# Optimization experiments

Hardware: AMD Instinct MI355X
Metric: run time of the kernel (lower is better)

The kernel has to match this reference:

```python
import jax, jax.numpy as jnp
from jax import lax
import numpy as np

B, T, F = 4096, 512, 63
NOINPUTS, HIDDEN, OUT = 64, 1024, 1  # NOINPUTS = F + OUT


def setup_inputs() -> dict:
    key = jax.random.key(0)
    k1, k2, k3, k4, k5, k6 = jax.random.split(key, 6)
    inputs = jax.random.normal(k1, (B, T, F), dtype=jnp.float32)
    labels = jax.random.normal(k2, (B, T, 1), dtype=jnp.float32)
    # FFNN params: Linear(noinputs, hidden) -> ReLU -> Linear(hidden, out)
    s1 = 1.0 / np.sqrt(NOINPUTS)
    s2 = 1.0 / np.sqrt(HIDDEN)
    W1 = jax.random.uniform(k3, (NOINPUTS, HIDDEN), jnp.float32, -s1, s1)
    b1 = jax.random.uniform(k4, (HIDDEN,), jnp.float32, -s1, s1)
    W2 = jax.random.uniform(k5, (HIDDEN, OUT), jnp.float32, -s2, s2)
    b2 = jax.random.uniform(k6, (OUT,), jnp.float32, -s2, s2)
    return {"inputs": inputs, "labels": labels, "W1": W1, "b1": b1, "W2": W2, "b2": b2}


def reference(inputs, labels, W1, b1, W2, b2):
    # output_size == 1 branch: result tensor starts as zeros (B,1,1);
    # each step feeds [inputs[:,t,:], last_pred] through the MLP.
    Bb = inputs.shape[0]

    def step(prev_pred, x_t):  # prev_pred: (B,1), x_t: (B,F)
        mi = jnp.concatenate([x_t, prev_pred], axis=1)      # (B, noinputs)
        h = jax.nn.relu(mi @ W1 + b1)                        # (B, hidden)
        pred = h @ W2 + b2                                   # (B, 1)
        return pred, pred

    xs = jnp.swapaxes(inputs[:, 1:, :], 0, 1)                # (T-1, B, F)
    init = jnp.zeros((Bb, 1), inputs.dtype)
    _, preds = lax.scan(step, init, xs)                      # (T-1, B, 1)
    preds = jnp.swapaxes(preds, 0, 1)                        # (B, T-1, 1)
    zero0 = jnp.zeros((Bb, 1, 1), inputs.dtype)
    return jnp.concatenate([zero0, preds], axis=1)           # (B, T, 1)
```

## Files before the change

### kernel.cpp

```cpp
#include <hip/hip_runtime.h>


#define TT 512
#define FF 63
#define HID 1024

typedef __attribute__((ext_vector_type(4))) float f32x4;
typedef __attribute__((ext_vector_type(4))) int i32x4;
typedef __attribute__((ext_vector_type(8))) _Float16 h16x8;

struct __attribute__((packed, aligned(4))) uf2 { float x, y; };

__device__ __forceinline__ void lds_barrier() {
  asm volatile("s_waitcnt lgkmcnt(0)" ::: "memory");
  __builtin_amdgcn_s_barrier();
  asm volatile("" ::: "memory");
}

__device__ __forceinline__ int pkh(float a, float b) {
  auto h = __builtin_amdgcn_cvt_pkrtz(fmaxf(a, 0.f), fmaxf(b, 0.f));
  return __builtin_bit_cast(int, h);
}
__device__ __forceinline__ int pk2h(float a, float b) {
  auto h = __builtin_amdgcn_cvt_pkrtz(a, b);
  return __builtin_bit_cast(int, h);
}

__global__ __launch_bounds__(512, 2)
void ffnn_ar_kernel(const float* __restrict__ x,
                    const float* __restrict__ W1,
                    const float* __restrict__ b1,
                    const float* __restrict__ W2,
                    const float* __restrict__ b2p,
                    float* __restrict__ out) {
  __shared__ __align__(16) _Float16 lds_A[2][16][72];
  __shared__ __align__(16) float lds_part[2][16][12];

  const int tid  = threadIdx.x;
  const int lane = tid & 63;
  const int w    = tid >> 6;
  const int c    = lane & 15;
  const int g    = lane >> 4;
  const int br   = blockIdx.x * 16;

  h16x8 bfr[8][2];
#pragma unroll
  for (int i = 0; i < 8; ++i) {
    const int n = (w * 8 + i) * 16 + c;
#pragma unroll
    for (int ks = 0; ks < 2; ++ks) {
      h16x8 f;
#pragma unroll
      for (int j = 0; j < 8; ++j) f[j] = (_Float16)W1[(ks * 32 + g * 8 + j) * HID + n];
      bfr[i][ks] = f;
    }
  }
  f32x4 b1v[8], w63v[8];
#pragma unroll
  for (int i = 0; i < 8; ++i) {
    const int nb = (w * 8 + i) * 16 + g * 4;
    b1v[i]  = (f32x4){b1[nb], b1[nb + 1], b1[nb + 2], b1[nb + 3]};
    w63v[i] = (f32x4){W1[63 * HID + nb], W1[63 * HID + nb + 1],
                      W1[63 * HID + nb + 2], W1[63 * HID + nb + 3]};
  }
  h16x8 a2f[4];
#pragma unroll
  for (int i2 = 0; i2 < 4; ++i2) {
    h16x8 f;
#pragma unroll
    for (int j = 0; j < 8; ++j)
      f[j] = (_Float16)W2[(w * 8 + 2 * i2 + (j >> 2)) * 16 + g * 4 + (j & 3)];
    a2f[i2] = f;
  }
  const float b2 = b2p[0];
  const float b2w = (w == 0) ? b2 : 0.f;

  const int srow = tid >> 5;
  const int sl   = tid & 31;
  const long rowbase = (long)(br + srow) * (TT * FF);
  const bool full = (sl < 31);

  {
    float xa, xb;
    if (full) { const uf2 v = *reinterpret_cast<const uf2*>(&x[rowbase + FF + 2 * sl]); xa = v.x; xb = v.y; }
    else      { xa = x[rowbase + FF + 62]; xb = 0.f; }
    *reinterpret_cast<int*>(&lds_A[1][srow][2 * sl]) = pk2h(xa, xb);
  }
  if (tid < 384) reinterpret_cast<float*>(lds_part)[tid] = 0.f;
  if (tid < 16) out[(long)(br + tid) * TT] = 0.f;

  float s0a, s0b, s1a, s1b;
  if (full) {
    const uf2 v0 = *reinterpret_cast<const uf2*>(&x[rowbase + 2 * FF + 2 * sl]);
    const uf2 v1 = *reinterpret_cast<const uf2*>(&x[rowbase + 3 * FF + 2 * sl]);
    s0a = v0.x; s0b = v0.y; s1a = v1.x; s1b = v1.y;
  } else {
    s0a = x[rowbase + 2 * FF + 62]; s0b = 0.f;
    s1a = x[rowbase + 3 * FF + 62]; s1b = 0.f;
  }

  lds_barrier();

#define STEP(T, CUR, SA, SB)                                                        \
  {                                                                                 \
         \
    const f32x4 v0 = *reinterpret_cast<const f32x4*>(&lds_part[(CUR) ^ 1][c][0]);   \
    const f32x4 v1 = *reinterpret_cast<const f32x4*>(&lds_part[(CUR) ^ 1][c][4]);   \
                   \
    const h16x8 xb0 = *reinterpret_cast<const h16x8*>(&lds_A[CUR][c][g * 8]);       \
    const h16x8 xb1 = *reinterpret_cast<const h16x8*>(&lds_A[CUR][c][32 + g * 8]);  \
    f32x4 acc[8];                                                                   \
    _Pragma("unroll") for (int i = 0; i < 8; ++i) {                                 \
      f32x4 z4 = __builtin_amdgcn_mfma_f32_16x16x32_f16(bfr[i][0], xb0, b1v[i], 0, 0, 0); \
      acc[i] = __builtin_amdgcn_mfma_f32_16x16x32_f16(bfr[i][1], xb1, z4, 0, 0, 0); \
    }                                                                               \
    const float pc = ((v0[0] + v0[1]) + (v0[2] + v0[3])) +                          \
                     ((v1[0] + v1[1]) + (v1[2] + v1[3]));                           \
    if (w == 0 && g == 0) out[(long)(br + c) * TT + ((T) - 1)] = pc;                \
     \
    *reinterpret_cast<int*>(&lds_A[(CUR) ^ 1][srow][2 * sl]) = pk2h(SA, SB);        \
    {                                                                               \
      const int tp = ((T) + 3 < TT) ? (T) + 3 : TT - 1;                             \
      if (full) { const uf2 v = *reinterpret_cast<const uf2*>(&x[rowbase + (long)tp * FF + 2 * sl]); \
                  SA = v.x; SB = v.y; }                                             \
      else      { SA = x[rowbase + (long)tp * FF + 62]; }                           \
    }                                                                               \
    \
    f32x4 p2a = {b2w, b2w, b2w, b2w};                                               \
    f32x4 p2b = {0.f, 0.f, 0.f, 0.f};                                               \
    f32x4 p2c = {0.f, 0.f, 0.f, 0.f};                                               \
    f32x4 p2d = {0.f, 0.f, 0.f, 0.f};                                               \
    _Pragma("unroll") for (int i2 = 0; i2 < 4; ++i2) {                              \
      const f32x4 u = acc[2 * i2], v = acc[2 * i2 + 1];                             \
      const f32x4 wu = w63v[2 * i2], wv = w63v[2 * i2 + 1];                         \
      const h16x8 hf = __builtin_bit_cast(h16x8, (i32x4){                           \
          pkh(fmaf(pc, wu[0], u[0]), fmaf(pc, wu[1], u[1])),                        \
          pkh(fmaf(pc, wu[2], u[2]), fmaf(pc, wu[3], u[3])),                        \
          pkh(fmaf(pc, wv[0], v[0]), fmaf(pc, wv[1], v[1])),                        \
          pkh(fmaf(pc, wv[2], v[2]), fmaf(pc, wv[3], v[3]))});                      \
      if (i2 == 0)      p2a = __builtin_amdgcn_mfma_f32_16x16x32_f16(a2f[0], hf, p2a, 0, 0, 0); \
      else if (i2 == 1) p2b = __builtin_amdgcn_mfma_f32_16x16x32_f16(a2f[1], hf, p2b, 0, 0, 0); \
      else if (i2 == 2) p2c = __builtin_amdgcn_mfma_f32_16x16x32_f16(a2f[2], hf, p2c, 0, 0, 0); \
      else              p2d = __builtin_amdgcn_mfma_f32_16x16x32_f16(a2f[3], hf, p2d, 0, 0, 0); \
    }                                                                               \
    if (g == 0) lds_part[CUR][c][w] = (p2a[0] + p2b[0]) + (p2c[0] + p2d[0]);        \
    lds_barrier();                                                                  \
  }

#pragma unroll 1
  for (int t = 1; t + 1 < TT; t += 2) {
    STEP(t, 1, s0a, s0b)
    STEP(t + 1, 0, s1a, s1b)
  }
  STEP(TT - 1, 1, s0a, s0b)

  {
    const f32x4 v0 = *reinterpret_cast<const f32x4*>(&lds_part[1][c][0]);
    const f32x4 v1 = *reinterpret_cast<const f32x4*>(&lds_part[1][c][4]);
    const float pc = ((v0[0] + v0[1]) + (v0[2] + v0[3])) +
                     ((v1[0] + v1[1]) + (v1[2] + v1[3]));
    if (w == 0 && g == 0) out[(long)(br + c) * TT + (TT - 1)] = pc;
  }
#undef STEP
}

extern "C" void kernel_launch(void* const* d_in, const int* in_sizes, int n_in,
                              void* d_out, int out_size, void* d_ws, size_t ws_size,
                              hipStream_t stream) {
  const float* x   = (const float*)d_in[0];
  const float* W1  = (const float*)d_in[2];
  const float* b1  = (const float*)d_in[3];
  const float* W2  = (const float*)d_in[4];
  const float* b2  = (const float*)d_in[5];
  float* out = (float*)d_out;

  ffnn_ar_kernel<<<256, 512, 0, stream>>>(x, W1, b1, W2, b2, out);
}
```

Before: 355.4 us.

## Software-pipeline the first-layer MFMA for the next step behind the recurrent tail

The input-dependent first-layer MFMAs for step t+1 are now issued at the end of step t, after the second-layer partials are written, so they overlap the barrier wait and the cross-wave reduction of the recurrent prediction. This requires a third LDS buffer for staged inputs, a deeper prefetch distance (t+4), and a 6-step unroll to rotate buffers. The ReLU/fma epilogue is also vectorised and the second-layer accumulation uses two chains instead of four, which shortens the serial dependency per step but adds register pressure from keeping acc live across the barrier.

```diff
diff --git a/kernel.cpp b/kernel.cpp
--- a/kernel.cpp
+++ b/kernel.cpp
@@ -17,10 +17,6 @@
   asm volatile("" ::: "memory");
 }
 
-__device__ __forceinline__ int pkh(float a, float b) {
-  auto h = __builtin_amdgcn_cvt_pkrtz(fmaxf(a, 0.f), fmaxf(b, 0.f));
-  return __builtin_bit_cast(int, h);
-}
 __device__ __forceinline__ int pk2h(float a, float b) {
   auto h = __builtin_amdgcn_cvt_pkrtz(a, b);
   return __builtin_bit_cast(int, h);
@@ -33,7 +29,7 @@
                     const float* __restrict__ W2,
                     const float* __restrict__ b2p,
                     float* __restrict__ out) {
-  __shared__ __align__(16) _Float16 lds_A[2][16][72];
+  __shared__ __align__(16) _Float16 lds_A[3][16][72];
   __shared__ __align__(16) float lds_part[2][16][12];
 
   const int tid  = threadIdx.x;
@@ -42,6 +38,7 @@
   const int c    = lane & 15;
   const int g    = lane >> 4;
   const int br   = blockIdx.x * 16;
+  const f32x4 zero4 = {0.f, 0.f, 0.f, 0.f};
 
   h16x8 bfr[8][2];
 #pragma unroll
@@ -81,84 +78,102 @@
   const bool full = (sl < 31);
 
   {
-    float xa, xb;
-    if (full) { const uf2 v = *reinterpret_cast<const uf2*>(&x[rowbase + FF + 2 * sl]); xa = v.x; xb = v.y; }
-    else      { xa = x[rowbase + FF + 62]; xb = 0.f; }
-    *reinterpret_cast<int*>(&lds_A[1][srow][2 * sl]) = pk2h(xa, xb);
+    float xa, xb2_;
+    if (full) { const uf2 v = *reinterpret_cast<const uf2*>(&x[rowbase + FF + 2 * sl]); xa = v.x; xb2_ = v.y; }
+    else      { xa = x[rowbase + FF + 62]; xb2_ = 0.f; }
+    *reinterpret_cast<int*>(&lds_A[1][srow][2 * sl]) = pk2h(xa, xb2_);
+    if (full) { const uf2 v = *reinterpret_cast<const uf2*>(&x[rowbase + 2 * FF + 2 * sl]); xa = v.x; xb2_ = v.y; }
+    else      { xa = x[rowbase + 2 * FF + 62]; xb2_ = 0.f; }
+    *reinterpret_cast<int*>(&lds_A[2][srow][2 * sl]) = pk2h(xa, xb2_);
   }
   if (tid < 384) reinterpret_cast<float*>(lds_part)[tid] = 0.f;
   if (tid < 16) out[(long)(br + tid) * TT] = 0.f;
 
-  float s0a, s0b, s1a, s1b;
+  float s0a = 0.f, s0b = 0.f, s1a = 0.f, s1b = 0.f;
   if (full) {
-    const uf2 v0 = *reinterpret_cast<const uf2*>(&x[rowbase + 2 * FF + 2 * sl]);
-    const uf2 v1 = *reinterpret_cast<const uf2*>(&x[rowbase + 3 * FF + 2 * sl]);
+    const uf2 v0 = *reinterpret_cast<const uf2*>(&x[rowbase + 3 * FF + 2 * sl]);
+    const uf2 v1 = *reinterpret_cast<const uf2*>(&x[rowbase + 4 * FF + 2 * sl]);
     s0a = v0.x; s0b = v0.y; s1a = v1.x; s1b = v1.y;
   } else {
-    s0a = x[rowbase + 2 * FF + 62]; s0b = 0.f;
-    s1a = x[rowbase + 3 * FF + 62]; s1b = 0.f;
+    s0a = x[rowbase + 3 * FF + 62];
+    s1a = x[rowbase + 4 * FF + 62];
   }
 
   lds_barrier();
 
-#define STEP(T, CUR, SA, SB)                                                        \
+  f32x4 acc[8];
+  {
+    const h16x8 nx0 = *reinterpret_cast<const h16x8*>(&lds_A[1][c][g * 8]);
+    const h16x8 nx1 = *reinterpret_cast<const h16x8*>(&lds_A[1][c][32 + g * 8]);
+#pragma unroll
+    for (int i = 0; i < 8; ++i) {
+      f32x4 z4 = __builtin_amdgcn_mfma_f32_16x16x32_f16(bfr[i][0], nx0, b1v[i], 0, 0, 0);
+      acc[i] = __builtin_amdgcn_mfma_f32_16x16x32_f16(bfr[i][1], nx1, z4, 0, 0, 0);
+    }
+  }
+
+#define STEP(T, ARD, AWR, PRD, PWR, SA, SB)                                         \
   {                                                                                 \
+    lds_barrier();                                                                  \
+       \
+    const f32x4 v0 = *reinterpret_cast<const f32x4*>(&lds_part[PRD][c][0]);         \
+    const f32x4 v1 = *reinterpret_cast<const f32x4*>(&lds_part[PRD][c][4]);         \
+                   \
+    const h16x8 nx0 = *reinterpret_cast<const h16x8*>(&lds_A[ARD][c][g * 8]);       \
+    const h16x8 nx1 = *reinterpret_cast<const h16x8*>(&lds_A[ARD][c][32 + g * 8]);  \
          \
-    const f32x4 v0 = *reinterpret_cast<const f32x4*>(&lds_part[(CUR) ^ 1][c][0]);   \
-    const f32x4 v1 = *reinterpret_cast<const f32x4*>(&lds_part[(CUR) ^ 1][c][4]);   \
-                   \
-    const h16x8 xb0 = *reinterpret_cast<const h16x8*>(&lds_A[CUR][c][g * 8]);       \
-    const h16x8 xb1 = *reinterpret_cast<const h16x8*>(&lds_A[CUR][c][32 + g * 8]);  \
-    f32x4 acc[8];                                                                   \
-    _Pragma("unroll") for (int i = 0; i < 8; ++i) {                                 \
-      f32x4 z4 = __builtin_amdgcn_mfma_f32_16x16x32_f16(bfr[i][0], xb0, b1v[i], 0, 0, 0); \
-      acc[i] = __builtin_amdgcn_mfma_f32_16x16x32_f16(bfr[i][1], xb1, z4, 0, 0, 0); \
-    }                                                                               \
-    const float pc = ((v0[0] + v0[1]) + (v0[2] + v0[3])) +                          \
-                     ((v1[0] + v1[1]) + (v1[2] + v1[3]));                           \
-    if (w == 0 && g == 0) out[(long)(br + c) * TT + ((T) - 1)] = pc;                \
-     \
-    *reinterpret_cast<int*>(&lds_A[(CUR) ^ 1][srow][2 * sl]) = pk2h(SA, SB);        \
+    *reinterpret_cast<int*>(&lds_A[AWR][srow][2 * sl]) = pk2h(SA, SB);              \
     {                                                                               \
-      const int tp = ((T) + 3 < TT) ? (T) + 3 : TT - 1;                             \
-      if (full) { const uf2 v = *reinterpret_cast<const uf2*>(&x[rowbase + (long)tp * FF + 2 * sl]); \
-                  SA = v.x; SB = v.y; }                                             \
+      const int tp = ((T) + 4 < TT) ? (T) + 4 : TT - 1;                             \
+      if (full) { const uf2 vv = *reinterpret_cast<const uf2*>(&x[rowbase + (long)tp * FF + 2 * sl]); \
+                  SA = vv.x; SB = vv.y; }                                           \
       else      { SA = x[rowbase + (long)tp * FF + 62]; }                           \
     }                                                                               \
-    \
+    const f32x4 sv = v0 + v1;                                                       \
+    const float pc = (sv[0] + sv[1]) + (sv[2] + sv[3]);                             \
+    if (w == 0 && g == 0) out[(long)(br + c) * TT + ((T) - 1)] = pc;                \
+    const f32x4 pc4 = {pc, pc, pc, pc};                                             \
+     \
     f32x4 p2a = {b2w, b2w, b2w, b2w};                                               \
     f32x4 p2b = {0.f, 0.f, 0.f, 0.f};                                               \
-    f32x4 p2c = {0.f, 0.f, 0.f, 0.f};                                               \
-    f32x4 p2d = {0.f, 0.f, 0.f, 0.f};                                               \
     _Pragma("unroll") for (int i2 = 0; i2 < 4; ++i2) {                              \
-      const f32x4 u = acc[2 * i2], v = acc[2 * i2 + 1];                             \
-      const f32x4 wu = w63v[2 * i2], wv = w63v[2 * i2 + 1];                         \
+      f32x4 zu = acc[2 * i2]     + pc4 * w63v[2 * i2];                              \
+      f32x4 zv = acc[2 * i2 + 1] + pc4 * w63v[2 * i2 + 1];                          \
+      zu = __builtin_elementwise_max(zu, zero4);                                    \
+      zv = __builtin_elementwise_max(zv, zero4);                                    \
       const h16x8 hf = __builtin_bit_cast(h16x8, (i32x4){                           \
-          pkh(fmaf(pc, wu[0], u[0]), fmaf(pc, wu[1], u[1])),                        \
-          pkh(fmaf(pc, wu[2], u[2]), fmaf(pc, wu[3], u[3])),                        \
-          pkh(fmaf(pc, wv[0], v[0]), fmaf(pc, wv[1], v[1])),                        \
-          pkh(fmaf(pc, wv[2], v[2]), fmaf(pc, wv[3], v[3]))});                      \
-      if (i2 == 0)      p2a = __builtin_amdgcn_mfma_f32_16x16x32_f16(a2f[0], hf, p2a, 0, 0, 0); \
-      else if (i2 == 1) p2b = __builtin_amdgcn_mfma_f32_16x16x32_f16(a2f[1], hf, p2b, 0, 0, 0); \
-      else if (i2 == 2) p2c = __builtin_amdgcn_mfma_f32_16x16x32_f16(a2f[2], hf, p2c, 0, 0, 0); \
-      else              p2d = __builtin_amdgcn_mfma_f32_16x16x32_f16(a2f[3], hf, p2d, 0, 0, 0); \
+          pk2h(zu[0], zu[1]), pk2h(zu[2], zu[3]),                                   \
+          pk2h(zv[0], zv[1]), pk2h(zv[2], zv[3])});                                 \
+      if (i2 & 1)                                                                   \
+        p2b = __builtin_amdgcn_mfma_f32_16x16x32_f16(a2f[i2], hf, p2b, 0, 0, 0);    \
+      else                                                                          \
+        p2a = __builtin_amdgcn_mfma_f32_16x16x32_f16(a2f[i2], hf, p2a, 0, 0, 0);    \
     }                                                                               \
-    if (g == 0) lds_part[CUR][c][w] = (p2a[0] + p2b[0]) + (p2c[0] + p2d[0]);        \
-    lds_barrier();                                                                  \
+    if (g == 0) lds_part[PWR][c][w] = p2a[0] + p2b[0];                              \
+           \
+    _Pragma("unroll") for (int i = 0; i < 8; ++i) {                                 \
+      f32x4 z4 = __builtin_amdgcn_mfma_f32_16x16x32_f16(bfr[i][0], nx0, b1v[i], 0, 0, 0); \
+      acc[i] = __builtin_amdgcn_mfma_f32_16x16x32_f16(bfr[i][1], nx1, z4, 0, 0, 0); \
+    }                                                                               \
   }
 
 #pragma unroll 1
-  for (int t = 1; t + 1 < TT; t += 2) {
-    STEP(t, 1, s0a, s0b)
-    STEP(t + 1, 0, s1a, s1b)
+  for (int t = 1; t + 5 < TT; t += 6) {
+    STEP(t + 0, 2, 0, 0, 1, s0a, s0b)
+    STEP(t + 1, 0, 1, 1, 0, s1a, s1b)
+    STEP(t + 2, 1, 2, 0, 1, s0a, s0b)
+    STEP(t + 3, 2, 0, 1, 0, s1a, s1b)
+    STEP(t + 4, 0, 1, 0, 1, s0a, s0b)
+    STEP(t + 5, 1, 2, 1, 0, s1a, s1b)
   }
-  STEP(TT - 1, 1, s0a, s0b)
+  STEP(TT - 1, 2, 0, 0, 1, s0a, s0b)
 
+  lds_barrier();
   {
     const f32x4 v0 = *reinterpret_cast<const f32x4*>(&lds_part[1][c][0]);
     const f32x4 v1 = *reinterpret_cast<const f32x4*>(&lds_part[1][c][4]);
-    const float pc = ((v0[0] + v0[1]) + (v0[2] + v0[3])) +
-                     ((v1[0] + v1[1]) + (v1[2] + v1[3]));
+    const f32x4 sv = v0 + v1;
+    const float pc = (sv[0] + sv[1]) + (sv[2] + sv[3]);
     if (w == 0 && g == 0) out[(long)(br + c) * TT + (TT - 1)] = pc;
   }
 #undef STEP
```

New measurement: 353.2 us. Within noise of the previous version (-0.6%).
